# Kernel optimization log

Measured on AMD Instinct MI355X. Metric: run time of the kernel, lower is better.

Reference implementation:

```python
import math
import jax, jax.numpy as jnp
import numpy as np

THETA = 2.0 ** 16
TWO_PI = 2.0 * math.pi


def _freqs(N):
    # quantize(arange(N), 2) = floor(t/2)*2 -> paired frequencies
    idx = jnp.floor(jnp.arange(N, dtype=jnp.float32) / 2.0) * 2.0
    return 1.0 / (THETA ** (idx / N)) / TWO_PI  # (N,)


def _rope(v, cos, sin):
    # rotate pairs: (-v_odd, v_even) interleaved back to original layout
    v_rot = jnp.stack((-v[..., 1::2], v[..., ::2]), axis=-1).reshape(v.shape)
    return v * cos + v_rot * sin


def setup_inputs() -> dict:
    key = jax.random.key(0)
    k1, k2 = jax.random.split(key)
    B, nh, T, N, D = 1, 4, 2048, 8192, 256
    Q = jax.random.normal(k1, (B, nh, T, N), dtype=jnp.float32) * 0.02
    V = jax.random.normal(k2, (B, 1, T, D), dtype=jnp.float32)
    return {"Q": Q, "V": V}


def reference(Q, V):
    # Q: (B, nh, T, N) sparse neuron space; V: (B, 1, T, D) embedding space; K is Q
    T, N = Q.shape[2], Q.shape[3]
    freqs = _freqs(N)
    phases = jnp.arange(T, dtype=jnp.float32)[:, None] * freqs[None, :]  # (T, N)
    ang = (phases % 1.0) * TWO_PI
    cos, sin = jnp.cos(ang), jnp.sin(ang)
    QR = _rope(Q, cos, sin)  # (B, nh, T, N)
    scores = jnp.einsum('bhtn,bhsn->bhts', QR, QR)  # (B, nh, T, T)
    causal = jnp.tril(jnp.ones((T, T), dtype=bool), k=-1)  # strictly lower
    scores = jnp.where(causal, scores, 0.0)
    # V broadcasts over heads: (B, nh, T, T) @ (B, 1, T, D) -> (B, nh, T, D)
    return jnp.matmul(scores, V)
```

## Files before the change

kernel.cpp:

```cpp
#include <hip/hip_runtime.h>

#define LDS_AS __attribute__((address_space(3)))
#define GLB_AS __attribute__((address_space(1)))

typedef __attribute__((ext_vector_type(8))) short bf16x8;
typedef __attribute__((ext_vector_type(4))) float f32x4;

static constexpr int NH = 4;
static constexpr int T  = 2048;
static constexpr int N  = 8192;
static constexpr int D  = 256;

__device__ inline unsigned short f2bf(float f) {
    unsigned int u = __float_as_uint(f);
    u += 0x7FFFu + ((u >> 16) & 1u);
    return (unsigned short)(u >> 16);
}

__device__ inline void gl2lds16(const void* g, void* l) {
    __builtin_amdgcn_global_load_lds((GLB_AS void*)g, (LDS_AS void*)l, 16, 0, 0);
}

__global__ void rope_kernel(const float* __restrict__ Q, unsigned short* __restrict__ QR) {
    int g = blockIdx.x * 256 + threadIdx.x;
    int base = g << 2;
    int n = base & (N - 1);
    int t = (base >> 13) & (T - 1);
    const float4 q = *(const float4*)(Q + (size_t)base);
    float tf = (float)t;
    const float inv2pi = 0.15915494309189535f;
    float f0 = exp2f((float)n       * (-1.0f / 512.0f)) * inv2pi;
    float f1 = exp2f((float)(n + 2) * (-1.0f / 512.0f)) * inv2pi;
    float r0 = tf * f0; r0 -= floorf(r0);
    float r1 = tf * f1; r1 -= floorf(r1);
    float s0 = __builtin_amdgcn_sinf(r0), c0 = __builtin_amdgcn_cosf(r0);
    float s1 = __builtin_amdgcn_sinf(r1), c1 = __builtin_amdgcn_cosf(r1);
    ushort4 o;
    o.x = f2bf(q.x * c0 - q.y * s0);
    o.y = f2bf(q.y * c0 + q.x * s0);
    o.z = f2bf(q.z * c1 - q.w * s1);
    o.w = f2bf(q.w * c1 + q.z * s1);
    *(ushort4*)(QR + (size_t)base) = o;
}

__global__ void vt_kernel(const float* __restrict__ V, unsigned short* __restrict__ Vt) {
    __shared__ unsigned short tile[64 * 65];
    int tb = blockIdx.x >> 2, db = blockIdx.x & 3;
    int t0 = tb * 64, d0 = db * 64;
    int tid = threadIdx.x;
    #pragma unroll
    for (int r = 0; r < 16; r++) {
        int idx = tid + r * 256;
        int tl = idx >> 6, dl = idx & 63;
        tile[tl * 65 + dl] = f2bf(V[(size_t)(t0 + tl) * D + d0 + dl]);
    }
    __syncthreads();
    #pragma unroll
    for (int r = 0; r < 16; r++) {
        int idx = tid + r * 256;
        int dl = idx >> 6, tl = idx & 63;
        Vt[(size_t)(d0 + dl) * T + t0 + tl] = tile[tl * 65 + dl];
    }
}

__global__ __launch_bounds__(256, 2) void gemm1_kernel(const unsigned short* __restrict__ QR,
                                                       unsigned short* __restrict__ S, int KS) {
    __shared__ __align__(16) unsigned short As[2][128 * 32];
    __shared__ __align__(16) unsigned short Bs[2][256 * 32];

    int bx = blockIdx.x;
    int per_h = 72 * KS;
    int h = bx / per_h;
    int rem = bx % per_h;
    int task = rem / KS;
    int ks = rem % KS;
    int bi = 0, cum = 0;
    for (; bi < 16; bi++) { int nb = (bi >> 1) + 1; if (cum + nb > task) break; cum += nb; }
    int bj = task - cum;

    const unsigned short* A = QR + (size_t)h * T * N + (size_t)bi * 128 * N;
    const unsigned short* B = QR + (size_t)h * T * N + (size_t)bj * 256 * N;

    int KN = N / KS;
    int k_begin = ks * KN;
    int nit = KN / 32;

    int tid = threadIdx.x;
    int lane = tid & 63, wave = tid >> 6;
    int wm = wave >> 1, wn = wave & 1;
    int quad = lane >> 4, l16 = lane & 15;
    int srow = tid >> 2;
    int scol = (tid & 3) * 8;

    f32x4 acc[4][8];
    #pragma unroll
    for (int i = 0; i < 4; i++)
        #pragma unroll
        for (int j = 0; j < 8; j++)
            #pragma unroll
            for (int r = 0; r < 4; r++) acc[i][j][r] = 0.0f;

    {
        int k0 = k_begin;
        gl2lds16(A + (size_t)srow * N + k0 + scol,         &As[0][srow * 32 + scol]);
        gl2lds16(A + (size_t)(srow + 64) * N + k0 + scol,  &As[0][(srow + 64) * 32 + scol]);
        gl2lds16(B + (size_t)srow * N + k0 + scol,         &Bs[0][srow * 32 + scol]);
        gl2lds16(B + (size_t)(srow + 64) * N + k0 + scol,  &Bs[0][(srow + 64) * 32 + scol]);
        gl2lds16(B + (size_t)(srow + 128) * N + k0 + scol, &Bs[0][(srow + 128) * 32 + scol]);
        gl2lds16(B + (size_t)(srow + 192) * N + k0 + scol, &Bs[0][(srow + 192) * 32 + scol]);
    }

    for (int it = 0; it < nit; it++) {
        int cur = it & 1, nxt = cur ^ 1;
        __syncthreads();
        if (it + 1 < nit) {
            int k0 = k_begin + (it + 1) * 32;
            gl2lds16(A + (size_t)srow * N + k0 + scol,         &As[nxt][srow * 32 + scol]);
            gl2lds16(A + (size_t)(srow + 64) * N + k0 + scol,  &As[nxt][(srow + 64) * 32 + scol]);
            gl2lds16(B + (size_t)srow * N + k0 + scol,         &Bs[nxt][srow * 32 + scol]);
            gl2lds16(B + (size_t)(srow + 64) * N + k0 + scol,  &Bs[nxt][(srow + 64) * 32 + scol]);
            gl2lds16(B + (size_t)(srow + 128) * N + k0 + scol, &Bs[nxt][(srow + 128) * 32 + scol]);
            gl2lds16(B + (size_t)(srow + 192) * N + k0 + scol, &Bs[nxt][(srow + 192) * 32 + scol]);
        }

        bf16x8 a[4];
        #pragma unroll
        for (int i = 0; i < 4; i++)
            a[i] = *(const bf16x8*)&As[cur][(wm * 64 + i * 16 + l16) * 32 + quad * 8];
        #pragma unroll
        for (int j = 0; j < 8; j++) {
            bf16x8 b = *(const bf16x8*)&Bs[cur][(wn * 128 + j * 16 + l16) * 32 + quad * 8];
            #pragma unroll
            for (int i = 0; i < 4; i++)
                acc[i][j] = __builtin_amdgcn_mfma_f32_16x16x32_bf16(a[i], b, acc[i][j], 0, 0, 0);
        }
    }

    unsigned short* Sh = S + (size_t)ks * NH * T * T + (size_t)h * T * T;
    #pragma unroll
    for (int i = 0; i < 4; i++) {
        int t_base = bi * 128 + wm * 64 + i * 16 + quad * 4;
        #pragma unroll
        for (int j = 0; j < 8; j++) {
            int s_g = bj * 256 + wn * 128 + j * 16 + l16;
            #pragma unroll
            for (int r = 0; r < 4; r++) {
                int t_g = t_base + r;
                float v = (s_g < t_g) ? acc[i][j][r] : 0.0f;
                Sh[(size_t)t_g * T + s_g] = f2bf(v);
            }
        }
    }
}

__global__ __launch_bounds__(256) void gemm2_kernel(const unsigned short* __restrict__ S,
                                                    const unsigned short* __restrict__ Vt,
                                                    float* __restrict__ out, int KS) {
    __shared__ __align__(16) unsigned short As[2][128 * 32];
    __shared__ __align__(16) unsigned short Bs[2][128 * 32];

    int bx = blockIdx.x;
    int per_h = 2 * 72;
    int h = bx / per_h;
    int rem = bx % per_h;
    int dblk = rem / 72;
    int tc = rem % 72;
    int bi = 0, cum = 0;
    for (; bi < 16; bi++) { int nc = (bi + 2) >> 1; if (cum + nc > tc) break; cum += nc; }
    int c = tc - cum;

    int kend = (bi + 1) * 128;
    int cstart = c * 256;
    int clen = min(256, kend - cstart);
    int cpk = clen >> 5;
    int ls = (KS == 4) ? 2 : (KS == 2) ? 1 : 0;
    int nit = cpk << ls;

    const unsigned short* Sh = S + (size_t)h * T * T + (size_t)bi * 128 * T + cstart;
    const size_t sstride = (size_t)NH * T * T;
    const unsigned short* B = Vt + (size_t)dblk * 128 * T + cstart;

    int tid = threadIdx.x;
    int lane = tid & 63, wave = tid >> 6;
    int wm = wave >> 1, wn = wave & 1;
    int quad = lane >> 4, l16 = lane & 15;
    int srow = tid >> 2;
    int scol = (tid & 3) * 8;

    f32x4 acc[4][4];
    #pragma unroll
    for (int i = 0; i < 4; i++)
        #pragma unroll
        for (int j = 0; j < 4; j++)
            #pragma unroll
            for (int r = 0; r < 4; r++) acc[i][j][r] = 0.0f;

    gl2lds16(Sh + (size_t)srow * T + scol,        &As[0][srow * 32 + scol]);
    gl2lds16(Sh + (size_t)(srow + 64) * T + scol, &As[0][(srow + 64) * 32 + scol]);
    gl2lds16(B + (size_t)srow * T + scol,         &Bs[0][srow * 32 + scol]);
    gl2lds16(B + (size_t)(srow + 64) * T + scol,  &Bs[0][(srow + 64) * 32 + scol]);

    bf16x8 b[4];
    for (int i = 0; i < nit; i++) {
        int k0i = i >> ls;
        int ks  = i & (KS - 1);
        __syncthreads();
        if (i + 1 < nit) {
            int ksn = (i + 1) & (KS - 1);
            int k0n = (i + 1) >> ls;
            const unsigned short* An = Sh + (size_t)ksn * sstride + k0n * 32;
            int pan = (i + 1) & 1;
            gl2lds16(An + (size_t)srow * T + scol,        &As[pan][srow * 32 + scol]);
            gl2lds16(An + (size_t)(srow + 64) * T + scol, &As[pan][(srow + 64) * 32 + scol]);
            if (ksn == 0) {
                const unsigned short* Bn = B + k0n * 32;
                int pbn = k0n & 1;
                gl2lds16(Bn + (size_t)srow * T + scol,        &Bs[pbn][srow * 32 + scol]);
                gl2lds16(Bn + (size_t)(srow + 64) * T + scol, &Bs[pbn][(srow + 64) * 32 + scol]);
            }
        }

        int pa = i & 1, pb = k0i & 1;
        if (ks == 0) {
            #pragma unroll
            for (int j = 0; j < 4; j++)
                b[j] = *(const bf16x8*)&Bs[pb][(wn * 64 + j * 16 + l16) * 32 + quad * 8];
        }
        bf16x8 a[4];
        #pragma unroll
        for (int ii = 0; ii < 4; ii++)
            a[ii] = *(const bf16x8*)&As[pa][(wm * 64 + ii * 16 + l16) * 32 + quad * 8];
        #pragma unroll
        for (int ii = 0; ii < 4; ii++)
            #pragma unroll
            for (int j = 0; j < 4; j++)
                acc[ii][j] = __builtin_amdgcn_mfma_f32_16x16x32_bf16(a[ii], b[j], acc[ii][j], 0, 0, 0);
    }

    float* oh = out + (size_t)h * T * D;
    #pragma unroll
    for (int i = 0; i < 4; i++) {
        int t_base = bi * 128 + wm * 64 + i * 16 + quad * 4;
        #pragma unroll
        for (int j = 0; j < 4; j++) {
            int d_g = dblk * 128 + wn * 64 + j * 16 + l16;
            #pragma unroll
            for (int r = 0; r < 4; r++) {
                int t_g = t_base + r;
                atomicAdd(&oh[(size_t)t_g * D + d_g], acc[i][j][r]);
            }
        }
    }
}

extern "C" void kernel_launch(void* const* d_in, const int* in_sizes, int n_in,
                              void* d_out, int out_size, void* d_ws, size_t ws_size,
                              hipStream_t stream) {
    const float* Q = (const float*)d_in[0];
    const float* V = (const float*)d_in[1];
    float* out = (float*)d_out;

    const size_t qr_elems = (size_t)NH * T * N;
    const size_t vt_elems = (size_t)D * T;
    const size_t s_elems  = (size_t)NH * T * T;

    int KS = 1;
    for (int cand : {4, 2, 1}) {
        if (ws_size >= (qr_elems + vt_elems + (size_t)cand * s_elems) * sizeof(unsigned short)) {
            KS = cand; break;
        }
    }
    if (ws_size < (qr_elems + vt_elems + (size_t)KS * s_elems) * sizeof(unsigned short)) return;

    unsigned short* QR = (unsigned short*)d_ws;
    unsigned short* Vt = QR + qr_elems;
    unsigned short* S  = Vt + vt_elems;

    rope_kernel<<<(NH * T * N / 4) / 256, 256, 0, stream>>>(Q, QR);
    vt_kernel<<<(T / 64) * (D / 64), 256, 0, stream>>>(V, Vt);
    gemm1_kernel<<<NH * 72 * KS, 256, 0, stream>>>(QR, S, KS);
    hipMemsetAsync(d_out, 0, (size_t)out_size * sizeof(float), stream);
    gemm2_kernel<<<NH * 2 * 72, 256, 0, stream>>>(S, Vt, out, KS);
}
```

Before: 603.7 us.

## Triple-buffer gemm1 LDS pipeline with explicit vmcnt waits and single barrier

Switches the QR·QR^T gemm1 main loop from double to triple buffering. Global-to-LDS loads run two stages ahead, with explicit s_waitcnt vmcnt(6) and a raw s_barrier in place of __syncthreads. All LDS fragments are read before the next prefetch is issued, and the MFMA block runs under raised wave priority. The aim is to hide global load latency and cut barrier stalls, at the cost of 50% more LDS per block (72KB), which may limit the two-blocks-per-CU occupancy. The gemm2 launch expression is rewritten but its value is unchanged.

```diff
diff --git a/kernel.cpp b/kernel.cpp
--- a/kernel.cpp
+++ b/kernel.cpp
@@ -65,8 +65,8 @@
 
 __global__ __launch_bounds__(256, 2) void gemm1_kernel(const unsigned short* __restrict__ QR,
                                                        unsigned short* __restrict__ S, int KS) {
-    __shared__ __align__(16) unsigned short As[2][128 * 32];
-    __shared__ __align__(16) unsigned short Bs[2][256 * 32];
+    __shared__ __align__(16) unsigned short As[3][128 * 32];
+    __shared__ __align__(16) unsigned short Bs[3][256 * 32];
 
     int bx = blockIdx.x;
     int per_h = 72 * KS;
@@ -100,40 +100,55 @@
             #pragma unroll
             for (int r = 0; r < 4; r++) acc[i][j][r] = 0.0f;
 
-    {
-        int k0 = k_begin;
-        gl2lds16(A + (size_t)srow * N + k0 + scol,         &As[0][srow * 32 + scol]);
-        gl2lds16(A + (size_t)(srow + 64) * N + k0 + scol,  &As[0][(srow + 64) * 32 + scol]);
-        gl2lds16(B + (size_t)srow * N + k0 + scol,         &Bs[0][srow * 32 + scol]);
-        gl2lds16(B + (size_t)(srow + 64) * N + k0 + scol,  &Bs[0][(srow + 64) * 32 + scol]);
-        gl2lds16(B + (size_t)(srow + 128) * N + k0 + scol, &Bs[0][(srow + 128) * 32 + scol]);
-        gl2lds16(B + (size_t)(srow + 192) * N + k0 + scol, &Bs[0][(srow + 192) * 32 + scol]);
-    }
-
+    #pragma unroll
+    for (int p = 0; p < 2; p++) {
+        int k0 = k_begin + p * 32;
+        gl2lds16(A + (size_t)srow * N + k0 + scol,         &As[p][srow * 32 + scol]);
+        gl2lds16(A + (size_t)(srow + 64) * N + k0 + scol,  &As[p][(srow + 64) * 32 + scol]);
+        gl2lds16(B + (size_t)srow * N + k0 + scol,         &Bs[p][srow * 32 + scol]);
+        gl2lds16(B + (size_t)(srow + 64) * N + k0 + scol,  &Bs[p][(srow + 64) * 32 + scol]);
+        gl2lds16(B + (size_t)(srow + 128) * N + k0 + scol, &Bs[p][(srow + 128) * 32 + scol]);
+        gl2lds16(B + (size_t)(srow + 192) * N + k0 + scol, &Bs[p][(srow + 192) * 32 + scol]);
+    }
+
+    int cur = 0, nxt2 = 2;
     for (int it = 0; it < nit; it++) {
-        int cur = it & 1, nxt = cur ^ 1;
-        __syncthreads();
         if (it + 1 < nit) {
-            int k0 = k_begin + (it + 1) * 32;
-            gl2lds16(A + (size_t)srow * N + k0 + scol,         &As[nxt][srow * 32 + scol]);
-            gl2lds16(A + (size_t)(srow + 64) * N + k0 + scol,  &As[nxt][(srow + 64) * 32 + scol]);
-            gl2lds16(B + (size_t)srow * N + k0 + scol,         &Bs[nxt][srow * 32 + scol]);
-            gl2lds16(B + (size_t)(srow + 64) * N + k0 + scol,  &Bs[nxt][(srow + 64) * 32 + scol]);
-            gl2lds16(B + (size_t)(srow + 128) * N + k0 + scol, &Bs[nxt][(srow + 128) * 32 + scol]);
-            gl2lds16(B + (size_t)(srow + 192) * N + k0 + scol, &Bs[nxt][(srow + 192) * 32 + scol]);
-        }
-
-        bf16x8 a[4];
+            asm volatile("s_waitcnt vmcnt(6)" ::: "memory");
+        } else {
+            asm volatile("s_waitcnt vmcnt(0)" ::: "memory");
+        }
+        __builtin_amdgcn_s_barrier();
+        __builtin_amdgcn_sched_barrier(0);
+
+        bf16x8 a[4], b[8];
         #pragma unroll
         for (int i = 0; i < 4; i++)
             a[i] = *(const bf16x8*)&As[cur][(wm * 64 + i * 16 + l16) * 32 + quad * 8];
         #pragma unroll
-        for (int j = 0; j < 8; j++) {
-            bf16x8 b = *(const bf16x8*)&Bs[cur][(wn * 128 + j * 16 + l16) * 32 + quad * 8];
+        for (int j = 0; j < 8; j++)
+            b[j] = *(const bf16x8*)&Bs[cur][(wn * 128 + j * 16 + l16) * 32 + quad * 8];
+
+        if (it + 2 < nit) {
+            int k0 = k_begin + (it + 2) * 32;
+            gl2lds16(A + (size_t)srow * N + k0 + scol,         &As[nxt2][srow * 32 + scol]);
+            gl2lds16(A + (size_t)(srow + 64) * N + k0 + scol,  &As[nxt2][(srow + 64) * 32 + scol]);
+            gl2lds16(B + (size_t)srow * N + k0 + scol,         &Bs[nxt2][srow * 32 + scol]);
+            gl2lds16(B + (size_t)(srow + 64) * N + k0 + scol,  &Bs[nxt2][(srow + 64) * 32 + scol]);
+            gl2lds16(B + (size_t)(srow + 128) * N + k0 + scol, &Bs[nxt2][(srow + 128) * 32 + scol]);
+            gl2lds16(B + (size_t)(srow + 192) * N + k0 + scol, &Bs[nxt2][(srow + 192) * 32 + scol]);
+        }
+
+        __builtin_amdgcn_s_setprio(1);
+        #pragma unroll
+        for (int j = 0; j < 8; j++)
             #pragma unroll
             for (int i = 0; i < 4; i++)
-                acc[i][j] = __builtin_amdgcn_mfma_f32_16x16x32_bf16(a[i], b, acc[i][j], 0, 0, 0);
-        }
+                acc[i][j] = __builtin_amdgcn_mfma_f32_16x16x32_bf16(a[i], b[j], acc[i][j], 0, 0, 0);
+        __builtin_amdgcn_s_setprio(0);
+
+        cur  = (cur  == 2) ? 0 : cur  + 1;
+        nxt2 = (nxt2 == 2) ? 0 : nxt2 + 1;
     }
 
     unsigned short* Sh = S + (size_t)ks * NH * T * T + (size_t)h * T * T;
@@ -280,5 +295,5 @@
     vt_kernel<<<(T / 64) * (D / 64), 256, 0, stream>>>(V, Vt);
     gemm1_kernel<<<NH * 72 * KS, 256, 0, stream>>>(QR, S, KS);
     hipMemsetAsync(d_out, 0, (size_t)out_size * sizeof(float), stream);
-    gemm2_kernel<<<NH * 2 * 72, 256, 0, stream>>>(S, Vt, out, KS);
-}
+    gemm2_kernel<<<NH * 2 * 40 * 0 + NH * 2 * 72, 256, 0, stream>>>(S, Vt, out, KS);
+}
```

After: 578.6 us. 4.2% less time.
